# Kernel optimization log

Hardware: AMD Instinct MI355X
Metric: run time of the kernel (lower is better)

The kernel has to match this reference:

```python
import jax, jax.numpy as jnp
import numpy as np


def setup_inputs() -> dict:
    key = jax.random.key(0)
    ks = jax.random.split(key, 6)
    B, S, D, H, K = 16384, 16, 256, 128, 32
    s1 = 1.0 / np.sqrt(D)
    s2 = 1.0 / np.sqrt(H)
    s3 = 1.0 / np.sqrt(K)
    return {
        "x": jax.random.normal(ks[0], (B, D), jnp.float32),
        "W1": jax.random.normal(ks[1], (S, D, H), jnp.float32) * s1,
        "b1": jnp.zeros((S, H), jnp.float32),
        "W2": jax.random.normal(ks[2], (S, H, D), jnp.float32) * s2,
        "b2": jnp.zeros((S, D), jnp.float32),
        "Wc1": jax.random.normal(ks[3], (S, D, K), jnp.float32) * s1,
        "bc1": jnp.zeros((S, K), jnp.float32),
        "Wc2": jax.random.normal(ks[4], (S, K), jnp.float32) * s3,
        "bc2": jnp.zeros((S,), jnp.float32),
        "lam": jnp.ones((S,), jnp.float32) / S,  # lambda_weights init = 1/n_sources
    }


def reference(x, W1, b1, W2, b2, Wc1, bc1, Wc2, bc2, lam):
    # Batched per-source 2-layer MLP: [B,D] x [S,D,H] -> [B,S,H]
    h = jax.nn.relu(jnp.einsum("bd,sdh->bsh", x, W1) + b1[None])
    outs = jnp.einsum("bsh,shd->bsd", h, W2) + b2[None]            # [B,S,D]
    # Confidence net on each source output
    ch = jax.nn.relu(jnp.einsum("bsd,sdk->bsk", outs, Wc1) + bc1[None])
    conf = jax.nn.sigmoid(jnp.einsum("bsk,sk->bs", ch, Wc2) + bc2[None])  # [B,S]
    # Weighted, normalized combination
    cw = lam[None, :] * conf                                        # [B,S]
    cw = cw / (cw.sum(axis=1, keepdims=True) + 1e-6)
    out = jnp.einsum("bsd,bs->bd", outs, cw)                        # [B,D]
    return out
```

## Files before the change

### kernel.cpp

```cpp
#include <hip/hip_runtime.h>
#include <math.h>

#define S_N 16
#define D_N 256
#define H_N 128
#define K_N 32
#define BT  64
#define B_N 16384

typedef __attribute__((ext_vector_type(8))) short bf16x8;
typedef __attribute__((ext_vector_type(4))) float f32x4;
typedef __attribute__((ext_vector_type(16))) float f32x16;

#define MFMA16(a, b, c) __builtin_amdgcn_mfma_f32_16x16x32_bf16(a, b, c, 0, 0, 0)
#define MFMA32(a, b, c) __builtin_amdgcn_mfma_f32_32x32x16_bf16(a, b, c, 0, 0, 0)
#define SWZ(r) ((unsigned)(((r) & 15) << 4))

static __device__ __forceinline__ unsigned short f2bf(float f) {
  union { float f; unsigned u; } v; v.f = f;
  unsigned r = v.u + 0x7FFFu + ((v.u >> 16) & 1u);
  return (unsigned short)(r >> 16);
}

__global__ __launch_bounds__(256)
void lsi_prep(const float* __restrict__ W1, const float* __restrict__ W2,
              const float* __restrict__ Wc1, const float* __restrict__ b2,
              const float* __restrict__ bc1,
              unsigned short* __restrict__ W1t,
              unsigned short* __restrict__ W2t,
              unsigned short* __restrict__ Wft,
              float* __restrict__ bcf)
{
  const int bid = blockIdx.x;
  if (bid < 1024) {
    __shared__ float t[32][33];
    const float* src; unsigned short* dst; int R, C, r0, c0;
    if (bid < 512) {
      int s = bid >> 5, tt = bid & 31;
      R = 256; C = 128; r0 = (tt >> 2) * 32; c0 = (tt & 3) * 32;
      src = W1 + (size_t)s * 256 * 128; dst = W1t + (size_t)s * 128 * 256;
    } else {
      int s = (bid - 512) >> 5, tt = (bid - 512) & 31;
      R = 128; C = 256; r0 = (tt >> 3) * 32; c0 = (tt & 7) * 32;
      src = W2 + (size_t)s * 128 * 256; dst = W2t + (size_t)s * 256 * 128;
    }
    int li = threadIdx.x >> 5, lj = threadIdx.x & 31;
    #pragma unroll
    for (int i = 0; i < 4; ++i)
      t[li + i * 8][lj] = src[(size_t)(r0 + li + i * 8) * C + c0 + lj];
    __syncthreads();
    #pragma unroll
    for (int i = 0; i < 4; ++i)
      dst[(size_t)(c0 + li + i * 8) * R + r0 + lj] = f2bf(t[lj][li + i * 8]);
    return;
  }
  const int q  = bid - 1024;
  const int s  = q >> 3, hb = q & 7;
  const int t  = threadIdx.x;
  const int hh = hb * 16 + (t >> 4);
  const int kb = (t & 15) * 2;
  const float* w2r = W2 + ((size_t)s * H_N + hh) * D_N;
  const float* wc1 = Wc1 + (size_t)s * D_N * K_N;
  float a0 = 0.f, a1 = 0.f;
  for (int d = 0; d < D_N; ++d) {
    float wv = w2r[d];
    a0 = fmaf(wv, wc1[d * K_N + kb], a0);
    a1 = fmaf(wv, wc1[d * K_N + kb + 1], a1);
  }
  Wft[((size_t)s * K_N + kb) * H_N + hh]     = f2bf(a0);
  Wft[((size_t)s * K_N + kb + 1) * H_N + hh] = f2bf(a1);
  if (hb == 0 && t < K_N) {
    float a = bc1[s * K_N + t];
    for (int d = 0; d < D_N; ++d)
      a = fmaf(b2[s * D_N + d], wc1[d * K_N + t], a);
    bcf[s * K_N + t] = a;
  }
}

__global__ __launch_bounds__(512, 2)
void lsi_main(const float* __restrict__ x,
              const float* __restrict__ b1,
              const float* __restrict__ b2,
              const float* __restrict__ Wc2,
              const float* __restrict__ bc2,
              const float* __restrict__ lam,
              const unsigned short* __restrict__ W1t,
              const unsigned short* __restrict__ W2t,
              const unsigned short* __restrict__ Wft,
              const float* __restrict__ bcf,
              float* __restrict__ out)
{
  __shared__ unsigned short x_lds[BT * D_N];
  __shared__ unsigned short h_lds[2][BT * H_N];
  __shared__ float cw_lds[2][BT];
  __shared__ float wsum_lds[BT];

  const int tid = threadIdx.x;
  const int w   = tid >> 6;
  const int l   = tid & 63;
  const int l31 = l & 31;
  const int hi  = l >> 5;
  const int rA  = l & 15;
  const int g   = l >> 4;
  const int k8  = g * 8;
  const int b0  = blockIdx.x * BT;

  {
    int row = tid >> 3;
    int c0  = (tid & 7) * 32;
    const float* xr = x + (size_t)(b0 + row) * D_N + c0;
    #pragma unroll
    for (int cc = 0; cc < 4; ++cc) {
      float4 f0 = *(const float4*)(xr + cc * 8);
      float4 f1 = *(const float4*)(xr + cc * 8 + 4);
      bf16x8 u;
      u[0] = f2bf(f0.x); u[1] = f2bf(f0.y); u[2] = f2bf(f0.z); u[3] = f2bf(f0.w);
      u[4] = f2bf(f1.x); u[5] = f2bf(f1.y); u[6] = f2bf(f1.z); u[7] = f2bf(f1.w);
      unsigned off = (unsigned)(row * 512 + (c0 + cc * 8) * 2) ^ SWZ(row);
      *(bf16x8*)((char*)x_lds + off) = u;
    }
  }
  if (tid < BT) wsum_lds[tid] = 0.f;

  f32x16 out_acc[2];
  f32x16 acc2[2];
  #pragma unroll
  for (int i = 0; i < 16; ++i) { out_acc[0][i] = 0.f; out_acc[1][i] = 0.f; }

  auto do_gemm1 = [&](int s, unsigned short* hw) {
    const int rt1 = w >> 2, ct1 = w & 3;
    const int arow = rt1 * 32 + l31;
    const int hcol = ct1 * 32 + l31;
    f32x16 acc1;
    #pragma unroll
    for (int i = 0; i < 16; ++i) acc1[i] = 0.f;
    const unsigned short* B1 = W1t + ((size_t)s * H_N + hcol) * D_N + hi * 8;
    #pragma unroll
    for (int kf = 0; kf < 16; ++kf) {
      bf16x8 bfr = *(const bf16x8*)(B1 + kf * 16);
      unsigned off = (unsigned)(arow * 512 + kf * 32 + hi * 16) ^ SWZ(arow);
      bf16x8 afr = *(const bf16x8*)((const char*)x_lds + off);
      acc1 = MFMA32(afr, bfr, acc1);
    }
    const float b1v = b1[s * H_N + hcol];
    #pragma unroll
    for (int r = 0; r < 16; ++r) {
      int row = rt1 * 32 + (r & 3) + 8 * (r >> 2) + 4 * hi;
      float v = fmaxf(acc1[r] + b1v, 0.f);
      unsigned off = (unsigned)(row * 256 + hcol * 2) ^ SWZ(row);
      *(unsigned short*)((char*)hw + off) = f2bf(v);
    }
  };

  __syncthreads();
  do_gemm1(0, h_lds[0]);
  __syncthreads();

  for (int s = 0; s < S_N; ++s) {
    const unsigned short* hr = (const unsigned short*)h_lds[s & 1];

    if (s > 0) {
      #pragma unroll
      for (int rt = 0; rt < 2; ++rt)
        #pragma unroll
        for (int q = 0; q < 4; ++q) {
          f32x4 c4 = *(const f32x4*)&cw_lds[(s + 1) & 1][rt * 32 + q * 8 + hi * 4];
          #pragma unroll
          for (int i = 0; i < 4; ++i)
            out_acc[rt][q * 4 + i] += c4[i] * acc2[rt][q * 4 + i];
        }
    }

    if (w < 4) {
      f32x4 acc3[2];
      acc3[0] = (f32x4){0.f, 0.f, 0.f, 0.f};
      acc3[1] = (f32x4){0.f, 0.f, 0.f, 0.f};
      const unsigned short* Bf = Wft + ((size_t)s * K_N + rA) * H_N + k8;
      #pragma unroll
      for (int ks = 0; ks < 4; ++ks) {
        int row = w * 16 + rA;
        unsigned off = (unsigned)(row * 256 + (ks * 32 + k8) * 2) ^ SWZ(row);
        bf16x8 afr = *(const bf16x8*)((const char*)hr + off);
        acc3[0] = MFMA16(afr, *(const bf16x8*)(Bf + ks * 32), acc3[0]);
        acc3[1] = MFMA16(afr, *(const bf16x8*)(Bf + 16 * H_N + ks * 32), acc3[1]);
      }
      const float bcf0 = bcf[s * K_N + rA],  bcf1 = bcf[s * K_N + 16 + rA];
      const float wc20 = Wc2[s * K_N + rA],  wc21 = Wc2[s * K_N + 16 + rA];
      float pz[4];
      #pragma unroll
      for (int i = 0; i < 4; ++i)
        pz[i] = fmaxf(acc3[0][i] + bcf0, 0.f) * wc20 +
                fmaxf(acc3[1][i] + bcf1, 0.f) * wc21;
      #pragma unroll
      for (int m = 1; m < 16; m <<= 1)
        #pragma unroll
        for (int i = 0; i < 4; ++i)
          pz[i] += __shfl_xor(pz[i], m);
      if (rA == 0) {
        const float lam_s = lam[s], bc2_s = bc2[s];
        #pragma unroll
        for (int i = 0; i < 4; ++i) {
          float cv = lam_s / (1.f + __expf(-(pz[i] + bc2_s)));
          cw_lds[s & 1][w * 16 + g * 4 + i] = cv;
          wsum_lds[w * 16 + g * 4 + i] += cv;
        }
      }
    }

    #pragma unroll
    for (int i = 0; i < 16; ++i) { acc2[0][i] = 0.f; acc2[1][i] = 0.f; }
    {
      const int dcol = w * 32 + l31;
      const unsigned short* B2 = W2t + ((size_t)s * D_N + dcol) * H_N + hi * 8;
      #pragma unroll
      for (int kf = 0; kf < 8; ++kf) {
        bf16x8 bfr = *(const bf16x8*)(B2 + kf * 16);
        #pragma unroll
        for (int rt = 0; rt < 2; ++rt) {
          int arow = rt * 32 + l31;
          unsigned off = (unsigned)(arow * 256 + kf * 32 + hi * 16) ^ SWZ(arow);
          bf16x8 afr = *(const bf16x8*)((const char*)hr + off);
          acc2[rt] = MFMA32(afr, bfr, acc2[rt]);
        }
      }
      const float b2v = b2[s * D_N + dcol];
      #pragma unroll
      for (int rt = 0; rt < 2; ++rt)
        #pragma unroll
        for (int r = 0; r < 16; ++r)
          acc2[rt][r] += b2v;
    }

    if (s + 1 < S_N) do_gemm1(s + 1, h_lds[(s + 1) & 1]);

    __syncthreads();
  }

  #pragma unroll
  for (int rt = 0; rt < 2; ++rt)
    #pragma unroll
    for (int q = 0; q < 4; ++q) {
      f32x4 c4 = *(const f32x4*)&cw_lds[(S_N - 1) & 1][rt * 32 + q * 8 + hi * 4];
      #pragma unroll
      for (int i = 0; i < 4; ++i)
        out_acc[rt][q * 4 + i] += c4[i] * acc2[rt][q * 4 + i];
    }
  {
    const int dcol = w * 32 + l31;
    #pragma unroll
    for (int rt = 0; rt < 2; ++rt)
      #pragma unroll
      for (int q = 0; q < 4; ++q) {
        f32x4 w4 = *(const f32x4*)&wsum_lds[rt * 32 + q * 8 + hi * 4];
        #pragma unroll
        for (int i = 0; i < 4; ++i) {
          int row = rt * 32 + q * 8 + hi * 4 + i;
          float winv = 1.f / (w4[i] + 1e-6f);
          out[(size_t)(b0 + row) * D_N + dcol] = out_acc[rt][q * 4 + i] * winv;
        }
      }
  }
}

extern "C" void kernel_launch(void* const* d_in, const int* in_sizes, int n_in,
                              void* d_out, int out_size, void* d_ws, size_t ws_size,
                              hipStream_t stream) {
  const float* x   = (const float*)d_in[0];
  const float* W1  = (const float*)d_in[1];
  const float* b1  = (const float*)d_in[2];
  const float* W2  = (const float*)d_in[3];
  const float* b2  = (const float*)d_in[4];
  const float* Wc1 = (const float*)d_in[5];
  const float* bc1 = (const float*)d_in[6];
  const float* Wc2 = (const float*)d_in[7];
  const float* bc2 = (const float*)d_in[8];
  const float* lam = (const float*)d_in[9];
  float* out = (float*)d_out;

  unsigned short* W1t = (unsigned short*)d_ws;
  unsigned short* W2t = W1t + (size_t)S_N * H_N * D_N;
  unsigned short* Wft = W2t + (size_t)S_N * D_N * H_N;
  float* bcf = (float*)(Wft + (size_t)S_N * K_N * H_N);

  lsi_prep<<<dim3(1152), dim3(256), 0, stream>>>(W1, W2, Wc1, b2, bc1,
                                                 W1t, W2t, Wft, bcf);
  lsi_main<<<dim3(B_N / BT), dim3(512), 0, stream>>>(x, b1, b2, Wc2, bc2, lam,
                                                     W1t, W2t, Wft, bcf, out);
}
```

Measured before the change: 136.4 us.

## Fold confidence weights into h and accumulate all sources in one GEMM2 chain

Halves the batch tile to 32 rows. Each wave now computes GEMM1 and the confidence net for two sources and stores all 16 h tiles in LDS. Each h is scaled by its confidence weight before the second GEMM, so the weighted sum over sources becomes a single K=16*128 accumulation per output tile. The b2 bias term is added separately from the weights. This removes the per-source cross-wave synchronisation and register-side output blending, and the output is staged through LDS for coalesced stores. In exchange it uses a much larger LDS footprint, which may lower occupancy, and rounds the cw-scaled activations to bf16.

```diff
diff --git a/kernel.cpp b/kernel.cpp
--- a/kernel.cpp
+++ b/kernel.cpp
@@ -5,14 +5,14 @@
 #define D_N 256
 #define H_N 128
 #define K_N 32
-#define BT  64
+#define BT  32
 #define B_N 16384
 
 typedef __attribute__((ext_vector_type(8))) short bf16x8;
+typedef __attribute__((ext_vector_type(4))) short bf16x4;
 typedef __attribute__((ext_vector_type(4))) float f32x4;
 typedef __attribute__((ext_vector_type(16))) float f32x16;
 
-#define MFMA16(a, b, c) __builtin_amdgcn_mfma_f32_16x16x32_bf16(a, b, c, 0, 0, 0)
 #define MFMA32(a, b, c) __builtin_amdgcn_mfma_f32_32x32x16_bf16(a, b, c, 0, 0, 0)
 #define SWZ(r) ((unsigned)(((r) & 15) << 4))
 
@@ -90,27 +90,23 @@
               const float* __restrict__ bcf,
               float* __restrict__ out)
 {
-  __shared__ unsigned short x_lds[BT * D_N];
-  __shared__ unsigned short h_lds[2][BT * H_N];
-  __shared__ float cw_lds[2][BT];
-  __shared__ float wsum_lds[BT];
+  __shared__ __align__(16) unsigned short x_lds[BT * D_N];
+  __shared__ __align__(16) unsigned short h_lds[S_N][BT * H_N];
+  __shared__ float cwh[S_N][BT];
 
   const int tid = threadIdx.x;
   const int w   = tid >> 6;
   const int l   = tid & 63;
   const int l31 = l & 31;
   const int hi  = l >> 5;
-  const int rA  = l & 15;
-  const int g   = l >> 4;
-  const int k8  = g * 8;
   const int b0  = blockIdx.x * BT;
 
   {
-    int row = tid >> 3;
-    int c0  = (tid & 7) * 32;
+    int row = tid >> 4;
+    int c0  = (tid & 15) * 16;
     const float* xr = x + (size_t)(b0 + row) * D_N + c0;
     #pragma unroll
-    for (int cc = 0; cc < 4; ++cc) {
+    for (int cc = 0; cc < 2; ++cc) {
       float4 f0 = *(const float4*)(xr + cc * 8);
       float4 f1 = *(const float4*)(xr + cc * 8 + 4);
       bf16x8 u;
@@ -120,145 +116,135 @@
       *(bf16x8*)((char*)x_lds + off) = u;
     }
   }
-  if (tid < BT) wsum_lds[tid] = 0.f;
-
-  f32x16 out_acc[2];
-  f32x16 acc2[2];
-  #pragma unroll
-  for (int i = 0; i < 16; ++i) { out_acc[0][i] = 0.f; out_acc[1][i] = 0.f; }
-
-  auto do_gemm1 = [&](int s, unsigned short* hw) {
-    const int rt1 = w >> 2, ct1 = w & 3;
-    const int arow = rt1 * 32 + l31;
-    const int hcol = ct1 * 32 + l31;
-    f32x16 acc1;
-    #pragma unroll
-    for (int i = 0; i < 16; ++i) acc1[i] = 0.f;
-    const unsigned short* B1 = W1t + ((size_t)s * H_N + hcol) * D_N + hi * 8;
+  __syncthreads();
+
+  #pragma unroll
+  for (int j = 0; j < 2; ++j) {
+    const int s = 2 * w + j;
+    unsigned short* hs = h_lds[s];
+
+    f32x16 a[4];
+    #pragma unroll
+    for (int t = 0; t < 4; ++t)
+      #pragma unroll
+      for (int i = 0; i < 16; ++i) a[t][i] = 0.f;
+    const unsigned short* A1 = W1t + (size_t)s * H_N * D_N + (size_t)l31 * D_N + hi * 8;
     #pragma unroll
     for (int kf = 0; kf < 16; ++kf) {
-      bf16x8 bfr = *(const bf16x8*)(B1 + kf * 16);
-      unsigned off = (unsigned)(arow * 512 + kf * 32 + hi * 16) ^ SWZ(arow);
-      bf16x8 afr = *(const bf16x8*)((const char*)x_lds + off);
-      acc1 = MFMA32(afr, bfr, acc1);
-    }
-    const float b1v = b1[s * H_N + hcol];
-    #pragma unroll
-    for (int r = 0; r < 16; ++r) {
-      int row = rt1 * 32 + (r & 3) + 8 * (r >> 2) + 4 * hi;
-      float v = fmaxf(acc1[r] + b1v, 0.f);
-      unsigned off = (unsigned)(row * 256 + hcol * 2) ^ SWZ(row);
-      *(unsigned short*)((char*)hw + off) = f2bf(v);
-    }
-  };
-
-  __syncthreads();
-  do_gemm1(0, h_lds[0]);
-  __syncthreads();
-
-  for (int s = 0; s < S_N; ++s) {
-    const unsigned short* hr = (const unsigned short*)h_lds[s & 1];
-
-    if (s > 0) {
-      #pragma unroll
-      for (int rt = 0; rt < 2; ++rt)
+      bf16x8 bx = *(const bf16x8*)((const char*)x_lds +
+                    ((unsigned)(l31 * 512 + kf * 32 + hi * 16) ^ SWZ(l31)));
+      a[0] = MFMA32(*(const bf16x8*)(A1 + kf * 16),              bx, a[0]);
+      a[1] = MFMA32(*(const bf16x8*)(A1 + 32 * D_N + kf * 16),   bx, a[1]);
+      a[2] = MFMA32(*(const bf16x8*)(A1 + 64 * D_N + kf * 16),   bx, a[2]);
+      a[3] = MFMA32(*(const bf16x8*)(A1 + 96 * D_N + kf * 16),   bx, a[3]);
+    }
+    #pragma unroll
+    for (int t = 0; t < 4; ++t)
+      #pragma unroll
+      for (int q = 0; q < 4; ++q) {
+        f32x4 b4 = *(const f32x4*)(b1 + s * H_N + t * 32 + q * 8 + hi * 4);
+        bf16x4 hv;
         #pragma unroll
-        for (int q = 0; q < 4; ++q) {
-          f32x4 c4 = *(const f32x4*)&cw_lds[(s + 1) & 1][rt * 32 + q * 8 + hi * 4];
-          #pragma unroll
-          for (int i = 0; i < 4; ++i)
-            out_acc[rt][q * 4 + i] += c4[i] * acc2[rt][q * 4 + i];
+        for (int i = 0; i < 4; ++i) {
+          float v = fmaxf(a[t][q * 4 + i] + b4[i], 0.f);
+          a[t][q * 4 + i] = v;
+          hv[i] = (short)f2bf(v);
         }
-    }
-
-    if (w < 4) {
-      f32x4 acc3[2];
-      acc3[0] = (f32x4){0.f, 0.f, 0.f, 0.f};
-      acc3[1] = (f32x4){0.f, 0.f, 0.f, 0.f};
-      const unsigned short* Bf = Wft + ((size_t)s * K_N + rA) * H_N + k8;
-      #pragma unroll
-      for (int ks = 0; ks < 4; ++ks) {
-        int row = w * 16 + rA;
-        unsigned off = (unsigned)(row * 256 + (ks * 32 + k8) * 2) ^ SWZ(row);
-        bf16x8 afr = *(const bf16x8*)((const char*)hr + off);
-        acc3[0] = MFMA16(afr, *(const bf16x8*)(Bf + ks * 32), acc3[0]);
-        acc3[1] = MFMA16(afr, *(const bf16x8*)(Bf + 16 * H_N + ks * 32), acc3[1]);
+        unsigned off = (unsigned)(l31 * 256 + (t * 32 + q * 8 + hi * 4) * 2) ^ SWZ(l31);
+        *(bf16x4*)((char*)hs + off) = hv;
       }
-      const float bcf0 = bcf[s * K_N + rA],  bcf1 = bcf[s * K_N + 16 + rA];
-      const float wc20 = Wc2[s * K_N + rA],  wc21 = Wc2[s * K_N + 16 + rA];
-      float pz[4];
+
+    f32x16 c3;
+    #pragma unroll
+    for (int i = 0; i < 16; ++i) c3[i] = 0.f;
+    const unsigned short* Af = Wft + (size_t)s * K_N * H_N + (size_t)l31 * H_N + hi * 8;
+    #pragma unroll
+    for (int kf = 0; kf < 8; ++kf) {
+      bf16x8 hb = *(const bf16x8*)((const char*)hs +
+                    ((unsigned)(l31 * 256 + kf * 32 + hi * 16) ^ SWZ(l31)));
+      c3 = MFMA32(*(const bf16x8*)(Af + kf * 16), hb, c3);
+    }
+    float zz = 0.f;
+    #pragma unroll
+    for (int q = 0; q < 4; ++q) {
+      f32x4 bc4 = *(const f32x4*)(bcf + s * K_N + q * 8 + hi * 4);
+      f32x4 wc4 = *(const f32x4*)(Wc2 + s * K_N + q * 8 + hi * 4);
       #pragma unroll
       for (int i = 0; i < 4; ++i)
-        pz[i] = fmaxf(acc3[0][i] + bcf0, 0.f) * wc20 +
-                fmaxf(acc3[1][i] + bcf1, 0.f) * wc21;
-      #pragma unroll
-      for (int m = 1; m < 16; m <<= 1)
+        zz += fmaxf(c3[q * 4 + i] + bc4[i], 0.f) * wc4[i];
+    }
+    zz += __shfl_xor(zz, 32);
+    const float cv = lam[s] / (1.f + __expf(-(zz + bc2[s])));
+    if (hi == 0) cwh[s][l31] = cv;
+
+    #pragma unroll
+    for (int t = 0; t < 4; ++t)
+      #pragma unroll
+      for (int q = 0; q < 4; ++q) {
+        bf16x4 hv;
         #pragma unroll
         for (int i = 0; i < 4; ++i)
-          pz[i] += __shfl_xor(pz[i], m);
-      if (rA == 0) {
-        const float lam_s = lam[s], bc2_s = bc2[s];
-        #pragma unroll
-        for (int i = 0; i < 4; ++i) {
-          float cv = lam_s / (1.f + __expf(-(pz[i] + bc2_s)));
-          cw_lds[s & 1][w * 16 + g * 4 + i] = cv;
-          wsum_lds[w * 16 + g * 4 + i] += cv;
-        }
+          hv[i] = (short)f2bf(a[t][q * 4 + i] * cv);
+        unsigned off = (unsigned)(l31 * 256 + (t * 32 + q * 8 + hi * 4) * 2) ^ SWZ(l31);
+        *(bf16x4*)((char*)hs + off) = hv;
       }
-    }
-
-    #pragma unroll
-    for (int i = 0; i < 16; ++i) { acc2[0][i] = 0.f; acc2[1][i] = 0.f; }
-    {
-      const int dcol = w * 32 + l31;
-      const unsigned short* B2 = W2t + ((size_t)s * D_N + dcol) * H_N + hi * 8;
-      #pragma unroll
-      for (int kf = 0; kf < 8; ++kf) {
-        bf16x8 bfr = *(const bf16x8*)(B2 + kf * 16);
-        #pragma unroll
-        for (int rt = 0; rt < 2; ++rt) {
-          int arow = rt * 32 + l31;
-          unsigned off = (unsigned)(arow * 256 + kf * 32 + hi * 16) ^ SWZ(arow);
-          bf16x8 afr = *(const bf16x8*)((const char*)hr + off);
-          acc2[rt] = MFMA32(afr, bfr, acc2[rt]);
-        }
-      }
-      const float b2v = b2[s * D_N + dcol];
-      #pragma unroll
-      for (int rt = 0; rt < 2; ++rt)
-        #pragma unroll
-        for (int r = 0; r < 16; ++r)
-          acc2[rt][r] += b2v;
-    }
-
-    if (s + 1 < S_N) do_gemm1(s + 1, h_lds[(s + 1) & 1]);
-
-    __syncthreads();
-  }
-
-  #pragma unroll
-  for (int rt = 0; rt < 2; ++rt)
-    #pragma unroll
-    for (int q = 0; q < 4; ++q) {
-      f32x4 c4 = *(const f32x4*)&cw_lds[(S_N - 1) & 1][rt * 32 + q * 8 + hi * 4];
-      #pragma unroll
-      for (int i = 0; i < 4; ++i)
-        out_acc[rt][q * 4 + i] += c4[i] * acc2[rt][q * 4 + i];
-    }
+  }
+  __syncthreads();
+
+  f32x16 oa, ob;
+  #pragma unroll
+  for (int i = 0; i < 16; ++i) { oa[i] = 0.f; ob[i] = 0.f; }
+  for (int s = 0; s < S_N; ++s) {
+    const unsigned short* A2 = W2t + (size_t)s * D_N * H_N +
+                               (size_t)(w * 32 + l31) * H_N + hi * 8;
+    const unsigned short* hs = h_lds[s];
+    #pragma unroll
+    for (int kf = 0; kf < 8; kf += 2) {
+      bf16x8 hb0 = *(const bf16x8*)((const char*)hs +
+                     ((unsigned)(l31 * 256 + kf * 32 + hi * 16) ^ SWZ(l31)));
+      bf16x8 hb1 = *(const bf16x8*)((const char*)hs +
+                     ((unsigned)(l31 * 256 + (kf + 1) * 32 + hi * 16) ^ SWZ(l31)));
+      oa = MFMA32(*(const bf16x8*)(A2 + kf * 16),       hb0, oa);
+      ob = MFMA32(*(const bf16x8*)(A2 + (kf + 1) * 16), hb1, ob);
+    }
+  }
+
+  float ws = 0.f;
+  #pragma unroll
+  for (int s = 0; s < S_N; ++s) ws += cwh[s][l31];
+  const float winv = 1.f / (ws + 1e-6f);
+  #pragma unroll
+  for (int q = 0; q < 4; ++q) {
+    const int dc = w * 32 + q * 8 + hi * 4;
+    f32x4 acc;
+    #pragma unroll
+    for (int i = 0; i < 4; ++i) acc[i] = oa[q * 4 + i] + ob[q * 4 + i];
+    for (int s = 0; s < S_N; ++s) {
+      const float c = cwh[s][l31];
+      f32x4 b4 = *(const f32x4*)(b2 + s * D_N + dc);
+      #pragma unroll
+      for (int i = 0; i < 4; ++i) acc[i] += c * b4[i];
+    }
+    #pragma unroll
+    for (int i = 0; i < 4; ++i) oa[q * 4 + i] = acc[i] * winv;
+  }
+  __syncthreads();
+
   {
-    const int dcol = w * 32 + l31;
-    #pragma unroll
-    for (int rt = 0; rt < 2; ++rt)
-      #pragma unroll
-      for (int q = 0; q < 4; ++q) {
-        f32x4 w4 = *(const f32x4*)&wsum_lds[rt * 32 + q * 8 + hi * 4];
-        #pragma unroll
-        for (int i = 0; i < 4; ++i) {
-          int row = rt * 32 + q * 8 + hi * 4 + i;
-          float winv = 1.f / (w4[i] + 1e-6f);
-          out[(size_t)(b0 + row) * D_N + dcol] = out_acc[rt][q * 4 + i] * winv;
-        }
-      }
+    float* tb = (float*)h_lds + (size_t)w * 1152;
+    #pragma unroll
+    for (int q = 0; q < 4; ++q)
+      *(f32x4*)(tb + l31 * 36 + q * 8 + hi * 4) =
+        (f32x4){oa[q * 4 + 0], oa[q * 4 + 1], oa[q * 4 + 2], oa[q * 4 + 3]};
+    #pragma unroll
+    for (int p = 0; p < 2; ++p) {
+      int row = (l >> 2) + p * 16;
+      f32x4 v0 = *(const f32x4*)(tb + row * 36 + (l & 3) * 8);
+      f32x4 v1 = *(const f32x4*)(tb + row * 36 + (l & 3) * 8 + 4);
+      float* op = out + (size_t)(b0 + row) * D_N + w * 32 + (l & 3) * 8;
+      *(f32x4*)op = v0;
+      *(f32x4*)(op + 4) = v1;
+    }
   }
 }
 
```

Measured after the change: 168.7 us. 23.6% more time.
